# Performance work log

Measured on AMD Instinct MI355X. Metric: run time of the kernel, lower is better.

The kernel has to match this reference:

```python
import jax, jax.numpy as jnp
import numpy as np

T, B, D_IN, D_HID, D_OUT = 256, 128, 512, 1024, 512


def setup_inputs() -> dict:
    key = jax.random.key(0)
    ks = jax.random.split(key, 7)
    s_i = 1.0 / np.sqrt(D_IN)
    s_h = 1.0 / np.sqrt(D_HID)
    return {
        "x": jax.random.normal(ks[0], (T, B, D_IN), jnp.float32),
        "Wi": jax.random.normal(ks[1], (D_HID, D_IN), jnp.float32) * s_i,
        "bi": jax.random.normal(ks[2], (D_HID,), jnp.float32) * s_i,
        "Wh": jax.random.normal(ks[3], (D_HID, D_HID), jnp.float32) * s_h,
        "bh": jax.random.normal(ks[4], (D_HID,), jnp.float32) * s_h,
        "Wo": jax.random.normal(ks[5], (D_OUT, D_HID), jnp.float32) * s_h,
        "bo": jax.random.normal(ks[6], (D_OUT,), jnp.float32) * s_h,
    }


def reference(x, Wi, bi, Wh, bh, Wo, bo):
    # Elman RNN: h_t = relu(x_t @ Wi^T + bi + h_{t-1} @ Wh^T + bh)
    # Precompute input projection for all timesteps (one big GEMM).
    zi = jnp.einsum("tbi,hi->tbh", x, Wi) + bi  # [T,B,H]

    def step(h, zi_t):
        z = jax.nn.relu(zi_t + h @ Wh.T + bh)
        return z, z

    h0 = jnp.zeros((x.shape[1], Wh.shape[0]), x.dtype)
    _, hidden = jax.lax.scan(step, h0, zi)  # hidden: [T,B,H]

    y = jnp.einsum("tbh,oh->tbo", hidden, Wo) + bo  # [T,B,O]
    hT = hidden[-1][None]  # [1,B,H]
    return hidden, hT, y
```

## Files before the change

kernel.cpp:

```cpp
#include <hip/hip_runtime.h>
#include <hip/hip_bf16.h>
#include <type_traits>

#define T_ 256
#define B_ 128
#define DIN_ 512
#define H_ 1024
#define DOUT_ 512

typedef __attribute__((ext_vector_type(8))) short bf16x8;
typedef __attribute__((ext_vector_type(4))) short s16x4;
typedef __attribute__((ext_vector_type(4))) float f32x4;
typedef unsigned long long u64;

__device__ inline short f2bf(float f) {
    return __builtin_bit_cast(short, __float2bfloat16(f));
}
__device__ inline float4 zload4(const short* p) {
    u64 u = *(const u64*)p;
    auto bf = [](unsigned x) { return __builtin_bit_cast(float, x << 16); };
    return make_float4(bf((unsigned)(u & 0xffff) ), bf((unsigned)((u >> 16) & 0xffff)),
                       bf((unsigned)((u >> 32) & 0xffff)), bf((unsigned)((u >> 48) & 0xffff)));
}
__device__ inline u64 pack4bf(float v0, float v1, float v2, float v3) {
    return (u64)(unsigned short)f2bf(v0)
         | ((u64)(unsigned short)f2bf(v1) << 16)
         | ((u64)(unsigned short)f2bf(v2) << 32)
         | ((u64)(unsigned short)f2bf(v3) << 48);
}

#define AT_LD64(p)    __hip_atomic_load((p), __ATOMIC_RELAXED, __HIP_MEMORY_SCOPE_AGENT)
#define AT_ST64(p, v) __hip_atomic_store((p), (v), __ATOMIC_RELAXED, __HIP_MEMORY_SCOPE_AGENT)

template <typename OUT_T>
__global__ __launch_bounds__(256)
void gemm_bias(const float* __restrict__ A, const float* __restrict__ W,
               const float* __restrict__ b1, const float* __restrict__ b2,
               OUT_T* __restrict__ out, int M, int N, int K)
{
    __shared__ short lA[4096];
    __shared__ short lB[4096];
    const int ntiles = N >> 7;
    const int bm = blockIdx.x / ntiles;
    const int bn = blockIdx.x % ntiles;
    const size_t m0 = (size_t)bm << 7;
    const size_t n0 = (size_t)bn << 7;
    const int tid = threadIdx.x;
    const int w = tid >> 6, l = tid & 63;
    const int wm = (w >> 1) << 6, wn = (w & 1) << 6;

    f32x4 acc[4][4] = {};
    float4 ra[4], rb[4];

    auto load_regs = [&](int k0) {
#pragma unroll
        for (int i = 0; i < 4; ++i) {
            int s = i * 256 + tid;
            int row = s >> 3, kq = s & 7;
            ra[i] = *(const float4*)(A + (m0 + row) * K + k0 + kq * 4);
            rb[i] = *(const float4*)(W + (n0 + row) * K + k0 + kq * 4);
        }
    };
    auto store_lds = [&]() {
#pragma unroll
        for (int i = 0; i < 4; ++i) {
            int s = i * 256 + tid;
            int row = s >> 3, kq = s & 7;
            int off = ((row >> 4) * 64 + ((row & 15) | ((kq >> 1) << 4))) * 8 + (kq & 1) * 4;
            s16x4 pa = { f2bf(ra[i].x), f2bf(ra[i].y), f2bf(ra[i].z), f2bf(ra[i].w) };
            s16x4 pb = { f2bf(rb[i].x), f2bf(rb[i].y), f2bf(rb[i].z), f2bf(rb[i].w) };
            *(s16x4*)&lA[off] = pa;
            *(s16x4*)&lB[off] = pb;
        }
    };

    load_regs(0);
    const int KI = K >> 5;
    for (int ki = 0; ki < KI; ++ki) {
        __syncthreads();
        store_lds();
        __syncthreads();
        if (ki + 1 < KI) load_regs((ki + 1) << 5);
        bf16x8 aF[4], bF[4];
#pragma unroll
        for (int i = 0; i < 4; ++i) {
            aF[i] = *(const bf16x8*)&lA[(((wm >> 4) + i) * 64 + l) * 8];
            bF[i] = *(const bf16x8*)&lB[(((wn >> 4) + i) * 64 + l) * 8];
        }
#pragma unroll
        for (int i = 0; i < 4; ++i)
#pragma unroll
            for (int j = 0; j < 4; ++j)
                acc[i][j] = __builtin_amdgcn_mfma_f32_16x16x32_bf16(aF[i], bF[j], acc[i][j], 0, 0, 0);
    }

#pragma unroll
    for (int j = 0; j < 4; ++j) {
        const int col = (int)n0 + wn + j * 16 + (l & 15);
        float bb = b1[col];
        if (b2) bb += b2[col];
#pragma unroll
        for (int i = 0; i < 4; ++i) {
#pragma unroll
            for (int r = 0; r < 4; ++r) {
                int row = (int)m0 + wm + i * 16 + (l >> 4) * 4 + r;
                float v = acc[i][j][r] + bb;
                if constexpr (std::is_same<OUT_T, short>::value)
                    out[(size_t)row * N + col] = f2bf(v);
                else
                    out[(size_t)row * N + col] = v;
            }
        }
    }
}

__global__ __launch_bounds__(256, 1)
void rnn_rec7(const short* __restrict__ zi, const float* __restrict__ Wh,
              float* __restrict__ hidden, unsigned short* __restrict__ hbuf)
{
    const int wg = blockIdx.x;
    const int bg = wg >> 4, cg = wg & 15;
    const int tid = threadIdx.x, w = tid >> 6, l = tid & 63;
    const int b = l & 15, hi = l >> 4;
    const int ocw = cg * 64 + w * 16;
    const u64 SIGN = 0x8000800080008000ull;

    __shared__ u64 lds_h[4096];

    bf16x8 wh[32];
#pragma unroll
    for (int kk = 0; kk < 32; ++kk) {
        const float* wp = Wh + (size_t)(ocw + b) * H_ + kk * 32 + hi * 8;
        float4 a = *(const float4*)wp;
        float4 c = *(const float4*)(wp + 4);
        bf16x8 v = { f2bf(a.x), f2bf(a.y), f2bf(a.z), f2bf(a.w),
                     f2bf(c.x), f2bf(c.y), f2bf(c.z), f2bf(c.w) };
        wh[kk] = v;
    }

    const int f0 = ocw + hi * 4;
    float4 z = zload4(zi + ((size_t)bg * 16 + b) * H_ + f0);

    const int kk2 = f0 >> 5, j0 = f0 & 7;
    const int lane2 = b | (((f0 >> 3) & 3) << 4);

#pragma unroll 1
    for (int t = 0; t < T_; ++t) {
        const size_t zb = (size_t)t * B_ * H_;
        f32x4 acc0 = {}, acc1 = {};
        if (t > 0) {
            const u64 expmask = (((t - 1) >> 1) & 1) ? SIGN : 0ull;
            const u64* hp = (const u64*)hbuf + (size_t)(((t + 1) & 1) * 8 + bg) * 4096;
            u64 sv[16];
#pragma unroll
            for (int i = 0; i < 16; ++i)
                sv[i] = AT_LD64(hp + i * 256 + tid);
            unsigned pend = 0xFFFFu;
            while (pend) {
#pragma unroll
                for (int i = 0; i < 16; ++i) {
                    if (pend & (1u << i)) {
                        if ((sv[i] & SIGN) == expmask) pend &= ~(1u << i);
                        else sv[i] = AT_LD64(hp + i * 256 + tid);
                    }
                }
            }
            if (expmask) {
#pragma unroll
                for (int i = 0; i < 16; ++i) sv[i] &= ~SIGN;
            }
#pragma unroll
            for (int i = 0; i < 16; ++i)
                lds_h[i * 256 + tid] = sv[i];
            __syncthreads();
#pragma unroll
            for (int kk = 0; kk < 32; ++kk) {
                bf16x8 hbf = *(const bf16x8*)&lds_h[(kk * 64 + l) * 2];
                if (kk & 1)
                    acc1 = __builtin_amdgcn_mfma_f32_16x16x32_bf16(wh[kk], hbf, acc1, 0, 0, 0);
                else
                    acc0 = __builtin_amdgcn_mfma_f32_16x16x32_bf16(wh[kk], hbf, acc0, 0, 0, 0);
            }
        }
        float v0 = fmaxf(acc0[0] + acc1[0] + z.x, 0.f);
        float v1 = fmaxf(acc0[1] + acc1[1] + z.y, 0.f);
        float v2 = fmaxf(acc0[2] + acc1[2] + z.z, 0.f);
        float v3 = fmaxf(acc0[3] + acc1[3] + z.w, 0.f);
        *(float4*)(hidden + zb + (size_t)(bg * 16 + b) * H_ + f0) =
            make_float4(v0, v1, v2, v3);
        unsigned short* hwS = hbuf + (size_t)((t & 1) * 8 + bg) * 16384;
        u64 payload = pack4bf(v0, v1, v2, v3) | (((t >> 1) & 1) ? SIGN : 0ull);
        AT_ST64((u64*)(hwS + (kk2 * 64 + lane2) * 8 + j0), payload);

        if (t + 1 < T_)
            z = zload4(zi + ((size_t)(t + 1) * B_ + bg * 16 + b) * H_ + f0);

        __syncthreads();
    }
}

__global__ __launch_bounds__(256)
void copy_k(const float4* __restrict__ s, float4* __restrict__ d)
{
    int i = blockIdx.x * 256 + threadIdx.x;
    d[i] = s[i];
}

extern "C" void kernel_launch(void* const* d_in, const int* in_sizes, int n_in,
                              void* d_out, int out_size, void* d_ws, size_t ws_size,
                              hipStream_t stream)
{
    const float* x  = (const float*)d_in[0];
    const float* Wi = (const float*)d_in[1];
    const float* bi = (const float*)d_in[2];
    const float* Wh = (const float*)d_in[3];
    const float* bh = (const float*)d_in[4];
    const float* Wo = (const float*)d_in[5];
    const float* bo = (const float*)d_in[6];

    float* hidden = (float*)d_out;
    float* hT     = hidden + (size_t)T_ * B_ * H_;
    float* y      = hT + (size_t)B_ * H_;

    const size_t HBUF_B = (size_t)2 * B_ * H_ * sizeof(short);
    const size_t ZI_B   = (size_t)T_ * B_ * H_ * sizeof(short);

    short* zi;
    unsigned short* hbuf;
    if (ws_size >= HBUF_B + ZI_B) {
        hbuf = (unsigned short*)d_ws;
        zi   = (short*)((char*)d_ws + HBUF_B);
    } else {
        zi   = (short*)y;
        hbuf = (unsigned short*)hT;
    }

    hipMemsetAsync(hbuf, 0xAA, HBUF_B, stream);

    gemm_bias<short><<<dim3(2048), dim3(256), 0, stream>>>(
        x, Wi, bi, bh, zi, T_ * B_, H_, DIN_);
    rnn_rec7<<<dim3(128), dim3(256), 0, stream>>>(zi, Wh, hidden, hbuf);

    copy_k<<<dim3(128), dim3(256), 0, stream>>>(
        (const float4*)(hidden + (size_t)(T_ - 1) * B_ * H_), (float4*)hT);

    gemm_bias<float><<<dim3(1024), dim3(256), 0, stream>>>(
        hidden, Wo, bo, nullptr, y, T_ * B_, DOUT_, H_);
}
```

Measured before the change: 1.033 ms.

## Consume hidden-state chunks directly from global memory with per-chunk spin waits

The recurrent kernel no longer gathers the whole previous hidden state into LDS behind a block-wide barrier. Each wave now polls and consumes 2-K-step chunks straight from global memory, staggered by column group, and feeds the MFMAs as soon as each chunk's sign-bit tags match. The aim is to overlap waiting on other workgroups with compute and to drop the __syncthreads per timestep. In exchange every wave issues its own redundant global loads, since the four waves read identical data, and the dependent load-then-MFMA chain is serialized with more polling traffic.

```diff
diff --git a/kernel.cpp b/kernel.cpp
--- a/kernel.cpp
+++ b/kernel.cpp
@@ -11,6 +11,7 @@
 typedef __attribute__((ext_vector_type(8))) short bf16x8;
 typedef __attribute__((ext_vector_type(4))) short s16x4;
 typedef __attribute__((ext_vector_type(4))) float f32x4;
+typedef __attribute__((ext_vector_type(2))) unsigned long long u64x2;
 typedef unsigned long long u64;
 
 __device__ inline short f2bf(float f) {
@@ -115,8 +116,8 @@
 }
 
 __global__ __launch_bounds__(256, 1)
-void rnn_rec7(const short* __restrict__ zi, const float* __restrict__ Wh,
-              float* __restrict__ hidden, unsigned short* __restrict__ hbuf)
+void rnn_rec10(const short* __restrict__ zi, const float* __restrict__ Wh,
+               float* __restrict__ hidden, unsigned short* __restrict__ hbuf)
 {
     const int wg = blockIdx.x;
     const int bg = wg >> 4, cg = wg & 15;
@@ -124,8 +125,6 @@
     const int b = l & 15, hi = l >> 4;
     const int ocw = cg * 64 + w * 16;
     const u64 SIGN = 0x8000800080008000ull;
-
-    __shared__ u64 lds_h[4096];
 
     bf16x8 wh[32];
 #pragma unroll
@@ -149,37 +148,27 @@
         const size_t zb = (size_t)t * B_ * H_;
         f32x4 acc0 = {}, acc1 = {};
         if (t > 0) {
-            const u64 expmask = (((t - 1) >> 1) & 1) ? SIGN : 0ull;
+            const u64 expm = (((t - 1) >> 1) & 1) ? SIGN : 0ull;
             const u64* hp = (const u64*)hbuf + (size_t)(((t + 1) & 1) * 8 + bg) * 4096;
-            u64 sv[16];
-#pragma unroll
-            for (int i = 0; i < 16; ++i)
-                sv[i] = AT_LD64(hp + i * 256 + tid);
-            unsigned pend = 0xFFFFu;
-            while (pend) {
-#pragma unroll
-                for (int i = 0; i < 16; ++i) {
-                    if (pend & (1u << i)) {
-                        if ((sv[i] & SIGN) == expmask) pend &= ~(1u << i);
-                        else sv[i] = AT_LD64(hp + i * 256 + tid);
-                    }
-                }
-            }
-            if (expmask) {
-#pragma unroll
-                for (int i = 0; i < 16; ++i) sv[i] &= ~SIGN;
-            }
-#pragma unroll
-            for (int i = 0; i < 16; ++i)
-                lds_h[i * 256 + tid] = sv[i];
-            __syncthreads();
-#pragma unroll
-            for (int kk = 0; kk < 32; ++kk) {
-                bf16x8 hbf = *(const bf16x8*)&lds_h[(kk * 64 + l) * 2];
-                if (kk & 1)
-                    acc1 = __builtin_amdgcn_mfma_f32_16x16x32_bf16(wh[kk], hbf, acc1, 0, 0, 0);
-                else
-                    acc0 = __builtin_amdgcn_mfma_f32_16x16x32_bf16(wh[kk], hbf, acc0, 0, 0, 0);
+#pragma unroll 1
+            for (int ci = 0; ci < 16; ++ci) {
+                const int c = (cg + ci) & 15;
+                const int ka = c * 2;
+                const u64* pa = hp + (ka * 64 + l) * 2;
+                const u64* pb = pa + 128;
+                u64 a0, a1, b0, b1;
+                do {
+                    a0 = AT_LD64(pa);     a1 = AT_LD64(pa + 1);
+                    b0 = AT_LD64(pb);     b1 = AT_LD64(pb + 1);
+                } while (!__all((int)(((a0 & SIGN) == expm) & ((a1 & SIGN) == expm) &
+                                      ((b0 & SIGN) == expm) & ((b1 & SIGN) == expm))));
+                if (expm) { a0 &= ~SIGN; a1 &= ~SIGN; b0 &= ~SIGN; b1 &= ~SIGN; }
+                u64x2 ua; ua.x = a0; ua.y = a1;
+                u64x2 ub; ub.x = b0; ub.y = b1;
+                acc0 = __builtin_amdgcn_mfma_f32_16x16x32_bf16(
+                           wh[ka], __builtin_bit_cast(bf16x8, ua), acc0, 0, 0, 0);
+                acc1 = __builtin_amdgcn_mfma_f32_16x16x32_bf16(
+                           wh[ka + 1], __builtin_bit_cast(bf16x8, ub), acc1, 0, 0, 0);
             }
         }
         float v0 = fmaxf(acc0[0] + acc1[0] + z.x, 0.f);
@@ -189,13 +178,11 @@
         *(float4*)(hidden + zb + (size_t)(bg * 16 + b) * H_ + f0) =
             make_float4(v0, v1, v2, v3);
         unsigned short* hwS = hbuf + (size_t)((t & 1) * 8 + bg) * 16384;
-        u64 payload = pack4bf(v0, v1, v2, v3) | (((t >> 1) & 1) ? SIGN : 0ull);
-        AT_ST64((u64*)(hwS + (kk2 * 64 + lane2) * 8 + j0), payload);
+        u64 pay = pack4bf(v0, v1, v2, v3) | (((t >> 1) & 1) ? SIGN : 0ull);
+        AT_ST64((u64*)(hwS + (kk2 * 64 + lane2) * 8 + j0), pay);
 
         if (t + 1 < T_)
             z = zload4(zi + ((size_t)(t + 1) * B_ + bg * 16 + b) * H_ + f0);
-
-        __syncthreads();
     }
 }
 
@@ -239,7 +226,7 @@
 
     gemm_bias<short><<<dim3(2048), dim3(256), 0, stream>>>(
         x, Wi, bi, bh, zi, T_ * B_, H_, DIN_);
-    rnn_rec7<<<dim3(128), dim3(256), 0, stream>>>(zi, Wh, hidden, hbuf);
+    rnn_rec10<<<dim3(128), dim3(256), 0, stream>>>(zi, Wh, hidden, hbuf);
 
     copy_k<<<dim3(128), dim3(256), 0, stream>>>(
         (const float4*)(hidden + (size_t)(T_ - 1) * B_ * H_), (float4*)hT);
```

New measurement: 2.331 ms. +125.6%, slower.
